# Optimization experiments

Measured on AMD Instinct MI355X. Metric: run time of the kernel, lower is better.

Reference implementation:

```python
import jax, jax.numpy as jnp
import numpy as np

OBJECTNESS_LIMIT = 0.7
MIN_SIZE = 10.0
N_ANCHORS = 9  # 3 aspects x 3 scales from RPN.anchors


def _conv(x, w, padding):
    return jax.lax.conv_general_dilated(
        x, w, window_strides=(1, 1), padding=padding,
        dimension_numbers=('NHWC', 'HWIO', 'NHWC'))


def setup_inputs() -> dict:
    key = jax.random.key(0)
    ks = jax.random.split(key, 7)
    B, H, W, C = 8, 64, 64, 512
    data = jax.random.normal(ks[0], (B, H, W, C), dtype=jnp.float32)
    # base 3x3 conv 512->256 ('normal' init), relu
    w_base = jax.random.normal(ks[1], (3, 3, C, 256), dtype=jnp.float32) * 0.05
    b_base = jnp.zeros((256,), dtype=jnp.float32)
    # classifier 1x1 conv 256->9 ('uniform' init), sigmoid
    w_cls = jax.random.uniform(ks[2], (1, 1, 256, N_ANCHORS), dtype=jnp.float32,
                               minval=-0.05, maxval=0.05)
    b_cls = jnp.zeros((N_ANCHORS,), dtype=jnp.float32)
    # branch is exercised / gradients flow)
    w_reg = jax.random.normal(ks[3], (1, 1, 256, N_ANCHORS * 4), dtype=jnp.float32) * 0.05
    b_reg = jnp.zeros((N_ANCHORS * 4,), dtype=jnp.float32)
    return {'data': data, 'w_base': w_base, 'b_base': b_base,
            'w_cls': w_cls, 'b_cls': b_cls, 'w_reg': w_reg, 'b_reg': b_reg}


def reference(data, w_base, b_base, w_cls, b_cls, w_reg, b_reg):
    # RPN base conv: 3x3, same padding, relu
    feat = jax.nn.relu(_conv(data, w_base, 'SAME') + b_base)        # [B,H,W,256]
    obj = jax.nn.sigmoid(_conv(feat, w_cls, 'VALID') + b_cls)       # [B,H,W,9]
    boxes = _conv(feat, w_reg, 'VALID') + b_reg                     # [B,H,W,36]
    B, H, W, _ = boxes.shape
    boxes = boxes.reshape(B, H, W, N_ANCHORS, 4)
    mask = (obj > OBJECTNESS_LIMIT) & (boxes[..., 2] > MIN_SIZE) & (boxes[..., 3] > MIN_SIZE)
    # boxes failing selection are dropped (yielded as None) -> zeroed here
    boxes = jnp.where(mask[..., None], boxes, jnp.zeros((), boxes.dtype))
    # objectness is always emitted; pack (boxes, objectness) densely
    out = jnp.concatenate([boxes.reshape(B, H, W, N_ANCHORS * 4), obj], axis=-1)  # [B,H,W,45]
    return out
```

## Files before the change

### kernel.cpp

```cpp
#include <hip/hip_runtime.h>
#include <hip/hip_bf16.h>

typedef unsigned short u16;
typedef unsigned int   u32;

typedef __attribute__((ext_vector_type(8))) short bfrag;
typedef __attribute__((ext_vector_type(4))) float f32x4;

static __device__ __forceinline__ u16 f2bf(float f) {
    u32 u = __float_as_uint(f);
    return (u16)((u + 0x7fffu + ((u >> 16) & 1u)) >> 16);
}
static __device__ __forceinline__ u32 pk2(float a, float b) {
    return (u32)f2bf(a) | ((u32)f2bf(b) << 16);
}
static __device__ __forceinline__ float bf2f(u16 h) {
    return __uint_as_float((u32)h << 16);
}

#define AS1 __attribute__((address_space(1)))
#define AS3 __attribute__((address_space(3)))
static __device__ __forceinline__ void gload_lds16(const u16* g, u16* l) {
    __builtin_amdgcn_global_load_lds((const AS1 u32*)g, (AS3 u32*)l, 16, 0, 0);
}

__global__ __launch_bounds__(256) void prep_all_k(
    const float* __restrict__ data,
    const float* __restrict__ wb,
    const float* __restrict__ wc,
    const float* __restrict__ wr,
    u16* __restrict__ abf,
    u16* __restrict__ wt,
    u16* __restrict__ wh)
{
    int b = blockIdx.x, tid = threadIdx.x;
    if (b < 8712) {
        int gid = b * 256 + tid;
        int ch8 = gid & 63;
        int row = gid >> 6;
        int img = row / 4356;
        int rem = row - img * 4356;
        int py  = rem / 66;
        int px  = rem - py * 66;
        uint4 o;
        if (py == 0 || py == 65 || px == 0 || px == 65) {
            o = make_uint4(0u, 0u, 0u, 0u);
        } else {
            const float4* s = (const float4*)(data +
                ((size_t)((img << 12) + ((py - 1) << 6) + (px - 1)) << 9) + (ch8 << 3));
            float4 v0 = s[0], v1 = s[1];
            o = make_uint4(pk2(v0.x, v0.y), pk2(v0.z, v0.w),
                           pk2(v1.x, v1.y), pk2(v1.z, v1.w));
        }
        *(uint4*)(abf + ((size_t)row << 9) + (ch8 << 3)) = o;
    } else if (b < 13320) {
        int i  = (b - 8712) * 256 + tid;
        int ci = i & 511;
        int co = (i >> 9) & 255;
        int pos = i >> 17;
        wt[i] = f2bf(wb[(size_t)((pos << 9) + ci) * 256 + co]);
    } else {
        int i = (b - 13320) * 256 + tid;
        int ch = i >> 8, c = i & 255;
        float v = 0.f;
        if (ch < 36)      v = wr[c * 36 + ch];
        else if (ch < 45) v = wc[c * 9 + ch - 36];
        wh[i] = f2bf(v);
    }
}

__global__ __launch_bounds__(256, 2) void gemm_k(
    const u16*   __restrict__ abf,
    const u16*   __restrict__ wt,
    const float* __restrict__ bb,
    u16*         __restrict__ feat)
{
    __shared__ u16 As[2][128 * 64];
    __shared__ u16 Bs[2][128 * 64];

    int bid = blockIdx.x;
    int wg  = ((bid & 7) << 6) | (bid >> 3);
    int mt  = wg >> 1, nt = wg & 1;
    int pm0 = mt << 7, cn0 = nt << 7;
    int img = mt >> 5;
    int y0  = (mt & 31) << 1;

    int tid = threadIdx.x, lane = tid & 63, w = tid >> 6;
    int wm2 = (w >> 1) << 6, wn2 = (w & 1) << 6;
    int fr = lane & 15, fg = lane >> 4;

    const u16* pA[4]; const u16* pB[4];
    int ldsOff[4];
    #pragma unroll
    for (int i = 0; i < 4; ++i) {
        int slot = i * 256 + w * 64 + lane;
        int row  = slot >> 3, g = slot & 7;
        int gs   = g ^ (row & 7);
        int y = y0 + (row >> 6), x = row & 63;
        pA[i] = abf + ((size_t)((img * 66 + y) * 66 + x) << 9) + (gs << 3);
        pB[i] = wt  + ((size_t)(cn0 + row) << 9) + (gs << 3);
        ldsOff[i] = (i * 256 + w * 64) << 3;
    }

    int aoff[2][4], boff[2][4];
    #pragma unroll
    for (int kk = 0; kk < 2; ++kk)
        #pragma unroll
        for (int t = 0; t < 4; ++t) {
            int ra = wm2 + (t << 4) + fr;
            int rb = wn2 + (t << 4) + fr;
            int q  = (kk << 2) | fg;
            aoff[kk][t] = (ra << 6) + ((q ^ (ra & 7)) << 3);
            boff[kk][t] = (rb << 6) + ((q ^ (rb & 7)) << 3);
        }

    f32x4 acc[4][4] = {};

    auto stage = [&](int s, int buf) {
        int kb  = s / 18;
        int rem = s - kb * 18;
        int pos = rem >> 1;
        int py  = pos / 3, px = pos - py * 3;
        size_t ko  = ((size_t)kb << 7) + ((size_t)(rem & 1) << 6);
        size_t soA = (((size_t)(py * 66 + px)) << 9) + ko;
        size_t soB = (((size_t)pos) << 17) + ko;
        u16* ad = &As[buf][0];
        u16* bd = &Bs[buf][0];
        #pragma unroll
        for (int i = 0; i < 4; ++i) gload_lds16(pA[i] + soA, ad + ldsOff[i]);
        #pragma unroll
        for (int i = 0; i < 4; ++i) gload_lds16(pB[i] + soB, bd + ldsOff[i]);
    };
    auto compute = [&](int buf) {
        const u16* a = &As[buf][0];
        const u16* b = &Bs[buf][0];
        #pragma unroll
        for (int kk = 0; kk < 2; ++kk) {
            bfrag av[4], bv[4];
            #pragma unroll
            for (int t = 0; t < 4; ++t) {
                av[t] = *(const bfrag*)(a + aoff[kk][t]);
                bv[t] = *(const bfrag*)(b + boff[kk][t]);
            }
            #pragma unroll
            for (int mi = 0; mi < 4; ++mi)
                #pragma unroll
                for (int ni = 0; ni < 4; ++ni)
                    acc[mi][ni] = __builtin_amdgcn_mfma_f32_16x16x32_bf16(
                        av[mi], bv[ni], acc[mi][ni], 0, 0, 0);
        }
    };

    stage(0, 0);
    __syncthreads();
    int cur = 0;
    #pragma unroll 1
    for (int s = 0; s < 72; ++s) {
        if (s < 71) stage(s + 1, cur ^ 1);
        compute(cur);
        __syncthreads();
        cur ^= 1;
    }

    #pragma unroll
    for (int ni = 0; ni < 4; ++ni) {
        int co = cn0 + wn2 + (ni << 4) + fr;
        float bias = bb[co];
        #pragma unroll
        for (int mi = 0; mi < 4; ++mi) {
            int pixb = pm0 + wm2 + (mi << 4) + (fg << 2);
            #pragma unroll
            for (int r = 0; r < 4; ++r) {
                float v = fmaxf(acc[mi][ni][r] + bias, 0.f);
                feat[(size_t)(pixb + r) * 256 + co] = f2bf(v);
            }
        }
    }
}

__global__ __launch_bounds__(256, 2) void head_k(
    const u16*   __restrict__ feat,
    const u16*   __restrict__ wh,
    const float* __restrict__ bc,
    const float* __restrict__ br,
    float*       __restrict__ out)
{
    __shared__ union {
        u16   ft[64 * 256];
        float raw[64 * 45];
    } sm;

    int bid = blockIdx.x;
    int wg  = ((bid & 7) << 6) | (bid >> 3);
    int pb  = wg << 6;

    int tid = threadIdx.x, lane = tid & 63, w = tid >> 6;
    int fr = lane & 15, fg = lane >> 4;
    int wm = w << 4;

    bfrag bv[3][8];
    #pragma unroll
    for (int nt = 0; nt < 3; ++nt)
        #pragma unroll
        for (int kk = 0; kk < 8; ++kk)
            bv[nt][kk] = *(const bfrag*)(wh + ((nt << 4) + fr) * 256 + (kk << 5) + (fg << 3));

    const u16* fbase = feat + ((size_t)pb << 8);
    #pragma unroll
    for (int i = 0; i < 8; ++i) {
        int slot = i * 256 + tid;
        int row  = slot >> 5, g = slot & 31;
        int gs   = g ^ (row & 7);
        gload_lds16(fbase + (row << 8) + (gs << 3), &sm.ft[(i * 256 + w * 64) << 3]);
    }
    __syncthreads();

    f32x4 acc[3] = {};
    #pragma unroll
    for (int kk = 0; kk < 8; ++kk) {
        int row = wm + fr;
        int ga  = (kk << 2) | fg;
        bfrag av = *(const bfrag*)&sm.ft[(row << 8) + ((ga ^ (row & 7)) << 3)];
        #pragma unroll
        for (int nt = 0; nt < 3; ++nt)
            acc[nt] = __builtin_amdgcn_mfma_f32_16x16x32_bf16(av, bv[nt][kk], acc[nt], 0, 0, 0);
    }
    __syncthreads();

    #pragma unroll
    for (int nt = 0; nt < 3; ++nt) {
        int ch = (nt << 4) + fr;
        if (ch < 45) {
            float bias = (ch < 36) ? br[ch] : bc[ch - 36];
            int pix = wm + (fg << 2);
            #pragma unroll
            for (int r = 0; r < 4; ++r)
                sm.raw[(pix + r) * 45 + ch] = acc[nt][r] + bias;
        }
    }
    __syncthreads();

    {
        int pix = tid >> 2, q = tid & 3;
        const float* rp = &sm.raw[pix * 45];
        float* op = out + (size_t)(pb + pix) * 45;
        int na = (q == 3) ? 3 : 2;
        int a0 = (q == 3) ? 6 : (q << 1);
        for (int t = 0; t < na; ++t) {
            int a = a0 + t;
            float lg  = rp[36 + a];
            float obj = 1.f / (1.f + __expf(-lg));
            float b0 = rp[4*a], b1 = rp[4*a+1], b2 = rp[4*a+2], b3 = rp[4*a+3];
            bool m = (obj > 0.7f) && (b2 > 10.f) && (b3 > 10.f);
            op[4*a    ] = m ? b0 : 0.f;
            op[4*a + 1] = m ? b1 : 0.f;
            op[4*a + 2] = m ? b2 : 0.f;
            op[4*a + 3] = m ? b3 : 0.f;
            op[36 + a ] = obj;
        }
    }
}

__global__ __launch_bounds__(256) void prep_w_k(const float* __restrict__ wb,
                                                u16* __restrict__ wt)
{
    int i  = blockIdx.x * 256 + threadIdx.x;
    int ci = i & 511;
    int co = (i >> 9) & 255;
    int pos = i >> 17;
    wt[i] = f2bf(wb[(size_t)((pos << 9) + ci) * 256 + co]);
}

union FbSmem {
    u16   hal[3 * 66 * 64];
    u16   ft[256][64];
    float raw[64 * 45];
};

template<int WMODE>
__global__ __launch_bounds__(256, 2) void fb_k(
    const float* __restrict__ data, const u16* __restrict__ wt,
    const float* __restrict__ wb, const float* __restrict__ bb,
    const float* __restrict__ wc, const float* __restrict__ bc,
    const float* __restrict__ wr, const float* __restrict__ br,
    float* __restrict__ out)
{
    __shared__ FbSmem sm;
    int bid = blockIdx.x;
    int wg  = ((bid & 7) << 6) | (bid >> 3);
    int pm0 = wg << 6;
    int img = wg >> 6;
    int y0  = wg & 63;
    int tid = threadIdx.x, lane = tid & 63, wid = tid >> 6;
    int wn = wid << 6;
    int fr = lane & 15, fg = lane >> 4;
    f32x4 acc[4][4] = {};

    #pragma unroll 1
    for (int cb = 0; cb < 8; ++cb) {
        __syncthreads();
        #pragma unroll
        for (int t = 0; t < 3; ++t) {
            int lin = t * 256 + tid;
            int row = lin >> 8, col = (lin >> 2) & 63, cq = lin & 3;
            int sy = y0 + row - 1;
            bool ok = (sy >= 0) && (sy < 64);
            float4 v0, v1, v2, v3;
            if (ok) {
                const float4* s = (const float4*)(data +
                    ((size_t)((img << 12) + (sy << 6) + col) << 9) + (cb << 6) + (cq << 4));
                v0 = s[0]; v1 = s[1]; v2 = s[2]; v3 = s[3];
            } else { v0 = v1 = v2 = v3 = make_float4(0.f, 0.f, 0.f, 0.f); }
            int hc = col + 1;
            u16* base = &sm.hal[(row * 66 + hc) << 6];
            int g0 = ((cq << 1) | 0) ^ (hc & 7);
            int g1 = ((cq << 1) | 1) ^ (hc & 7);
            *(uint4*)&base[g0 << 3] = make_uint4(pk2(v0.x,v0.y), pk2(v0.z,v0.w),
                                                 pk2(v1.x,v1.y), pk2(v1.z,v1.w));
            *(uint4*)&base[g1 << 3] = make_uint4(pk2(v2.x,v2.y), pk2(v2.z,v2.w),
                                                 pk2(v3.x,v3.y), pk2(v3.z,v3.w));
        }
        if (tid < 48) {
            int zr = tid >> 4, zrem = tid & 15;
            int zc = (zrem >> 3) ? 65 : 0, zg = zrem & 7;
            *(uint4*)&sm.hal[(((zr * 66 + zc) << 3) | zg) << 3] = make_uint4(0,0,0,0);
        }
        __syncthreads();

        #pragma unroll
        for (int pos = 0; pos < 9; ++pos) {
            int dy = pos / 3 - 1, dx = pos % 3 - 1;
            bfrag bv[2][4];
            if (WMODE == 0) {
                #pragma unroll
                for (int kk = 0; kk < 2; ++kk)
                    #pragma unroll
                    for (int i = 0; i < 4; ++i)
                        bv[kk][i] = *(const bfrag*)(wt + ((size_t)pos << 17) +
                            ((size_t)(wn + (i << 4) + fr) << 9) + (cb << 6) +
                            (kk << 5) + (fg << 3));
            } else {
                #pragma unroll
                for (int kk = 0; kk < 2; ++kk)
                    #pragma unroll
                    for (int i = 0; i < 4; ++i) {
                        int co = wn + (i << 4) + fr;
                        const float* s = wb +
                            (size_t)((pos << 9) + (cb << 6) + (kk << 5) + (fg << 3)) * 256 + co;
                        union { short sh[8]; bfrag v; } tb;
                        #pragma unroll
                        for (int j = 0; j < 8; ++j) tb.sh[j] = (short)f2bf(s[(size_t)j << 8]);
                        bv[kk][i] = tb.v;
                    }
            }
            int hr = dy + 1;
            bfrag av[2][4];
            #pragma unroll
            for (int kk = 0; kk < 2; ++kk)
                #pragma unroll
                for (int i = 0; i < 4; ++i) {
                    int hc = (i << 4) + fr + dx + 1;
                    int g  = ((kk << 2) | fg) ^ (hc & 7);
                    av[kk][i] = *(const bfrag*)&sm.hal[(((hr * 66 + hc) << 3) | g) << 3];
                }
            #pragma unroll
            for (int kk = 0; kk < 2; ++kk)
                #pragma unroll
                for (int mi = 0; mi < 4; ++mi)
                    #pragma unroll
                    for (int ni = 0; ni < 4; ++ni)
                        acc[mi][ni] = __builtin_amdgcn_mfma_f32_16x16x32_bf16(
                            av[kk][mi], bv[kk][ni], acc[mi][ni], 0, 0, 0);
        }
    }
    __syncthreads();

    #pragma unroll
    for (int ni = 0; ni < 4; ++ni) {
        int co = wn + (ni << 4) + fr;
        float bias = bb[co];
        int rot = (co & 15) << 2;
        #pragma unroll
        for (int mi = 0; mi < 4; ++mi) {
            int pb  = (mi << 4) + (fg << 2);
            int col = (pb + rot) & 63;
            float r0 = fmaxf(acc[mi][ni][0] + bias, 0.f);
            float r1 = fmaxf(acc[mi][ni][1] + bias, 0.f);
            float r2 = fmaxf(acc[mi][ni][2] + bias, 0.f);
            float r3 = fmaxf(acc[mi][ni][3] + bias, 0.f);
            *(uint2*)&sm.ft[co][col] = make_uint2(pk2(r0, r1), pk2(r2, r3));
        }
    }
    __syncthreads();

    int wchx = __builtin_amdgcn_readfirstlane(wid) * 12;
    float a12[12];
    #pragma unroll
    for (int j = 0; j < 12; ++j) {
        int ch = wchx + j;
        a12[j] = (ch < 36) ? br[ch] : ((ch < 45) ? bc[ch - 36] : 0.f);
    }
    #pragma unroll 4
    for (int c = 0; c < 256; ++c) {
        int col = (lane + ((c & 15) << 2)) & 63;
        float f = bf2f(sm.ft[c][col]);
        #pragma unroll
        for (int j = 0; j < 12; ++j) {
            int ch = wchx + j;
            if (ch < 36)      a12[j] = fmaf(f, wr[c * 36 + ch], a12[j]);
            else if (ch < 45) a12[j] = fmaf(f, wc[c * 9 + ch - 36], a12[j]);
        }
    }
    __syncthreads();
    #pragma unroll
    for (int j = 0; j < 12; ++j) {
        int ch = wchx + j;
        if (ch < 45) sm.raw[lane * 45 + ch] = a12[j];
    }
    __syncthreads();
    {
        int pix = tid >> 2, q = tid & 3;
        const float* rp = &sm.raw[pix * 45];
        float* op = out + (size_t)(pm0 + pix) * 45;
        int na = (q == 3) ? 3 : 2;
        int a0 = (q == 3) ? 6 : (q << 1);
        for (int t = 0; t < na; ++t) {
            int a = a0 + t;
            float lg  = rp[36 + a];
            float obj = 1.f / (1.f + __expf(-lg));
            float b0 = rp[4*a], b1 = rp[4*a+1], b2 = rp[4*a+2], b3 = rp[4*a+3];
            bool m = (obj > 0.7f) && (b2 > 10.f) && (b3 > 10.f);
            op[4*a    ] = m ? b0 : 0.f;
            op[4*a + 1] = m ? b1 : 0.f;
            op[4*a + 2] = m ? b2 : 0.f;
            op[4*a + 3] = m ? b3 : 0.f;
            op[36 + a ] = obj;
        }
    }
}

extern "C" void kernel_launch(void* const* d_in, const int* in_sizes, int n_in,
                              void* d_out, int out_size, void* d_ws, size_t ws_size,
                              hipStream_t stream)
{
    const float* data = (const float*)d_in[0];
    const float* wb   = (const float*)d_in[1];
    const float* bb   = (const float*)d_in[2];
    const float* wc   = (const float*)d_in[3];
    const float* bcl  = (const float*)d_in[4];
    const float* wr   = (const float*)d_in[5];
    const float* brg  = (const float*)d_in[6];
    float* out = (float*)d_out;

    const size_t ABF_B  = (size_t)8 * 66 * 66 * 512 * 2;
    const size_t WT_B   = (size_t)9 * 256 * 512 * 2;
    const size_t FEAT_B = (size_t)32768 * 256 * 2;
    const size_t WH_B   = (size_t)64 * 256 * 2;

    if (ws_size >= ABF_B + WT_B + FEAT_B + WH_B) {
        u16* abf  = (u16*)d_ws;
        u16* wt   = (u16*)((char*)d_ws + ABF_B);
        u16* feat = (u16*)((char*)d_ws + ABF_B + WT_B);
        u16* wh   = (u16*)((char*)d_ws + ABF_B + WT_B + FEAT_B);
        prep_all_k<<<13384, 256, 0, stream>>>(data, wb, wc, wr, abf, wt, wh);
        gemm_k<<<512, 256, 0, stream>>>(abf, wt, bb, feat);
        head_k<<<512, 256, 0, stream>>>(feat, wh, bcl, brg, out);
    } else if (ws_size >= WT_B) {
        u16* wt = (u16*)d_ws;
        prep_w_k<<<4608, 256, 0, stream>>>(wb, wt);
        fb_k<0><<<512, 256, 0, stream>>>(data, wt, wb, bb, wc, bcl, wr, brg, out);
    } else {
        fb_k<1><<<512, 256, 0, stream>>>(data, (const u16*)nullptr, wb,
                                         bb, wc, bcl, wr, brg, out);
    }
}
```

Baseline: 110.2 us.

## Widen GEMM tile to full N with 8 waves and triple-buffered LDS pipeline

The conv GEMM now uses 512-thread blocks that each cover 128 pixels by all 256 output channels, so A tiles are loaded once instead of twice. LDS grows to three stages with prefetch two steps ahead, and partial vmcnt waits replace full syncs. Split barriers and setprio interleave the LDS reads with MFMA bursts. The grid halves to 256 blocks and LDS use rises to about 144KB, so occupancy falls to one block per CU and there may be fewer blocks than CUs.

Result: slower. 117.2 us (+6.4%).

```diff
diff --git a/kernel.cpp b/kernel.cpp
--- a/kernel.cpp
+++ b/kernel.cpp
@@ -69,37 +69,43 @@
     }
 }
 
-__global__ __launch_bounds__(256, 2) void gemm_k(
+__global__ __launch_bounds__(512, 2) void gemm_k(
     const u16*   __restrict__ abf,
     const u16*   __restrict__ wt,
     const float* __restrict__ bb,
     u16*         __restrict__ feat)
 {
-    __shared__ u16 As[2][128 * 64];
-    __shared__ u16 Bs[2][128 * 64];
+    __shared__ u16 As[3][128 * 64];
+    __shared__ u16 Bs[3][256 * 64];
 
     int bid = blockIdx.x;
-    int wg  = ((bid & 7) << 6) | (bid >> 3);
-    int mt  = wg >> 1, nt = wg & 1;
-    int pm0 = mt << 7, cn0 = nt << 7;
-    int img = mt >> 5;
-    int y0  = (mt & 31) << 1;
-
-    int tid = threadIdx.x, lane = tid & 63, w = tid >> 6;
-    int wm2 = (w >> 1) << 6, wn2 = (w & 1) << 6;
+    int wg  = ((bid & 7) << 5) | (bid >> 3);
+    int pm0 = wg << 7;
+    int img = wg >> 5;
+    int y0  = (wg & 31) << 1;
+
+    int tid = threadIdx.x, lane = tid & 63, wid = tid >> 6;
+    int wm2 = (wid >> 2) << 6, wn2 = (wid & 3) << 6;
     int fr = lane & 15, fg = lane >> 4;
 
-    const u16* pA[4]; const u16* pB[4];
-    int ldsOff[4];
-    #pragma unroll
-    for (int i = 0; i < 4; ++i) {
-        int slot = i * 256 + w * 64 + lane;
+    const u16* pA[2]; const u16* pB[4];
+    int aLds[2], bLds[4];
+    #pragma unroll
+    for (int i = 0; i < 2; ++i) {
+        int slot = i * 512 + tid;
         int row  = slot >> 3, g = slot & 7;
         int gs   = g ^ (row & 7);
-        int y = y0 + (row >> 6), x = row & 63;
-        pA[i] = abf + ((size_t)((img * 66 + y) * 66 + x) << 9) + (gs << 3);
-        pB[i] = wt  + ((size_t)(cn0 + row) << 9) + (gs << 3);
-        ldsOff[i] = (i * 256 + w * 64) << 3;
+        pA[i]   = abf + ((size_t)((img * 66 + y0 + (row >> 6)) * 66 + (row & 63)) << 9)
+                      + (gs << 3);
+        aLds[i] = slot << 3;
+    }
+    #pragma unroll
+    for (int i = 0; i < 4; ++i) {
+        int slot = i * 512 + tid;
+        int row  = slot >> 3, g = slot & 7;
+        int gs   = g ^ (row & 7);
+        pB[i]   = wt + ((size_t)row << 9) + (gs << 3);
+        bLds[i] = slot << 3;
     }
 
     int aoff[2][4], boff[2][4];
@@ -116,9 +122,9 @@
 
     f32x4 acc[4][4] = {};
 
-    auto stage = [&](int s, int buf) {
-        int kb  = s / 18;
-        int rem = s - kb * 18;
+    auto stage = [&](int t, int buf) {
+        int kb  = t / 18;
+        int rem = t - kb * 18;
         int pos = rem >> 1;
         int py  = pos / 3, px = pos - py * 3;
         size_t ko  = ((size_t)kb << 7) + ((size_t)(rem & 1) << 6);
@@ -127,44 +133,73 @@
         u16* ad = &As[buf][0];
         u16* bd = &Bs[buf][0];
         #pragma unroll
-        for (int i = 0; i < 4; ++i) gload_lds16(pA[i] + soA, ad + ldsOff[i]);
-        #pragma unroll
-        for (int i = 0; i < 4; ++i) gload_lds16(pB[i] + soB, bd + ldsOff[i]);
+        for (int i = 0; i < 2; ++i) gload_lds16(pA[i] + soA, ad + aLds[i]);
+        #pragma unroll
+        for (int i = 0; i < 4; ++i) gload_lds16(pB[i] + soB, bd + bLds[i]);
     };
-    auto compute = [&](int buf) {
-        const u16* a = &As[buf][0];
-        const u16* b = &Bs[buf][0];
-        #pragma unroll
-        for (int kk = 0; kk < 2; ++kk) {
+
+    stage(0, 0);
+    stage(1, 1);
+    asm volatile("s_waitcnt vmcnt(6)" ::: "memory");
+    __builtin_amdgcn_sched_barrier(0);
+    __builtin_amdgcn_s_barrier();
+
+    int b = 0;
+    #pragma unroll 1
+    for (int t = 0; t < 72; ++t) {
+        int b2 = b + 2; if (b2 >= 3) b2 -= 3;
+        const u16* a = &As[b][0];
+        const u16* bp = &Bs[b][0];
+
+        {
             bfrag av[4], bv[4];
             #pragma unroll
-            for (int t = 0; t < 4; ++t) {
-                av[t] = *(const bfrag*)(a + aoff[kk][t]);
-                bv[t] = *(const bfrag*)(b + boff[kk][t]);
+            for (int i = 0; i < 4; ++i) {
+                av[i] = *(const bfrag*)(a  + aoff[0][i]);
+                bv[i] = *(const bfrag*)(bp + boff[0][i]);
             }
+            if (t + 2 < 72) stage(t + 2, b2);
+            __builtin_amdgcn_s_barrier();
+            __builtin_amdgcn_s_setprio(1);
             #pragma unroll
             for (int mi = 0; mi < 4; ++mi)
                 #pragma unroll
                 for (int ni = 0; ni < 4; ++ni)
                     acc[mi][ni] = __builtin_amdgcn_mfma_f32_16x16x32_bf16(
                         av[mi], bv[ni], acc[mi][ni], 0, 0, 0);
-        }
-    };
-
-    stage(0, 0);
-    __syncthreads();
-    int cur = 0;
-    #pragma unroll 1
-    for (int s = 0; s < 72; ++s) {
-        if (s < 71) stage(s + 1, cur ^ 1);
-        compute(cur);
-        __syncthreads();
-        cur ^= 1;
+            __builtin_amdgcn_s_setprio(0);
+            __builtin_amdgcn_s_barrier();
+        }
+        {
+            bfrag av[4], bv[4];
+            #pragma unroll
+            for (int i = 0; i < 4; ++i) {
+                av[i] = *(const bfrag*)(a  + aoff[1][i]);
+                bv[i] = *(const bfrag*)(bp + boff[1][i]);
+            }
+            __builtin_amdgcn_s_barrier();
+            __builtin_amdgcn_s_setprio(1);
+            #pragma unroll
+            for (int mi = 0; mi < 4; ++mi)
+                #pragma unroll
+                for (int ni = 0; ni < 4; ++ni)
+                    acc[mi][ni] = __builtin_amdgcn_mfma_f32_16x16x32_bf16(
+                        av[mi], bv[ni], acc[mi][ni], 0, 0, 0);
+            __builtin_amdgcn_s_setprio(0);
+            if (t < 70) {
+                asm volatile("s_waitcnt vmcnt(6)" ::: "memory");
+            } else {
+                asm volatile("s_waitcnt vmcnt(0)" ::: "memory");
+            }
+            __builtin_amdgcn_sched_barrier(0);
+            __builtin_amdgcn_s_barrier();
+        }
+        b = (b == 2) ? 0 : b + 1;
     }
 
     #pragma unroll
     for (int ni = 0; ni < 4; ++ni) {
-        int co = cn0 + wn2 + (ni << 4) + fr;
+        int co = wn2 + (ni << 4) + fr;
         float bias = bb[co];
         #pragma unroll
         for (int mi = 0; mi < 4; ++mi) {
@@ -463,7 +498,7 @@
         u16* feat = (u16*)((char*)d_ws + ABF_B + WT_B);
         u16* wh   = (u16*)((char*)d_ws + ABF_B + WT_B + FEAT_B);
         prep_all_k<<<13384, 256, 0, stream>>>(data, wb, wc, wr, abf, wt, wh);
-        gemm_k<<<512, 256, 0, stream>>>(abf, wt, bb, feat);
+        gemm_k<<<256, 512, 0, stream>>>(abf, wt, bb, feat);
         head_k<<<512, 256, 0, stream>>>(feat, wh, bcl, brg, out);
     } else if (ws_size >= WT_B) {
         u16* wt = (u16*)d_ws;
```
